# Kernel optimization log

Measured on AMD Instinct MI355X. Metric: run time of the kernel, lower is better.

## Reference

```python
import jax, jax.numpy as jnp
import numpy as np

N, C_IN, C_OUT, H, W = 64, 128, 128, 64, 64
K, RED = 3, 16


def setup_inputs() -> dict:
    key = jax.random.key(0)
    ks = jax.random.split(key, 12)
    s = 0.02
    return {
        "x": jax.random.normal(ks[0], (N, C_IN, H, W), dtype=jnp.float32),
        # spatial_extractor: Linear(16 -> 9)
        "W_sp": jax.random.normal(ks[1], (16, K * K), dtype=jnp.float32) * s,
        "b_sp": jnp.zeros((K * K,), dtype=jnp.float32),
        # out_channel_extractor: Linear(C_IN -> C_OUT//RED) -> ReLU -> Linear(-> C_OUT)
        "W_o1": jax.random.normal(ks[2], (C_IN, C_OUT // RED), dtype=jnp.float32) * s,
        "b_o1": jnp.zeros((C_OUT // RED,), dtype=jnp.float32),
        "W_o2": jax.random.normal(ks[3], (C_OUT // RED, C_OUT), dtype=jnp.float32) * s,
        "b_o2": jnp.zeros((C_OUT,), dtype=jnp.float32),
        # in_channel_extractor: Linear(C_IN -> C_IN//RED) -> ReLU -> Linear(-> C_IN)
        "W_i1": jax.random.normal(ks[4], (C_IN, C_IN // RED), dtype=jnp.float32) * s,
        "b_i1": jnp.zeros((C_IN // RED,), dtype=jnp.float32),
        "W_i2": jax.random.normal(ks[5], (C_IN // RED, C_IN), dtype=jnp.float32) * s,
        "b_i2": jnp.zeros((C_IN,), dtype=jnp.float32),
    }


def reference(x, W_sp, b_sp, W_o1, b_o1, W_o2, b_o2, W_i1, b_i1, W_i2, b_i2):
    n, c, h, w = x.shape
    # AdaptiveAvgPool2d(4): H,W divisible by 4 -> exact 16x16 mean pooling
    xs = x.reshape(n, c, 4, h // 4, 4, w // 4).mean(axis=(3, 5))  # [n,c,4,4]
    xs = xs.reshape(n, c, 16).mean(axis=1)                        # [n,16]
    sp = (xs @ W_sp + b_sp).reshape(n, K, K)                      # [n,3,3]
    gap = x.mean(axis=(2, 3))                                     # [n,C_in]
    co = jax.nn.relu(gap @ W_o1 + b_o1) @ W_o2 + b_o2             # [n,C_out]
    ci = jax.nn.relu(gap @ W_i1 + b_i1) @ W_i2 + b_i2             # [n,C_in]
    # per-sample kernel: [n, C_out, C_in, K, K]
    weight = (co[:, :, None, None, None] * ci[:, None, :, None, None]
              * sp[:, None, None, :, :])

    def per_sample_conv(xi, wi):
        # xi: [C_in,H,W], wi: [C_out,C_in,K,K]
        return jax.lax.conv_general_dilated(
            xi[None], wi, window_strides=(1, 1),
            padding=[(1, 1), (1, 1)])[0]

    return jax.vmap(per_sample_conv)(x, weight)  # [n,C_out,H,W]
```

## Files before the change

kernel.cpp:

```cpp
#include <hip/hip_runtime.h>

#define NB   64
#define CIN  128
#define COUT 128
#define HH   64
#define WW   64
#define HW   4096
#define HID  8


__global__ __launch_bounds__(256) void k_blocksums(const float* __restrict__ x,
                                                   float* __restrict__ bs) {
    const int plane = blockIdx.x;
    const int tid = threadIdx.x;
    const int r = tid >> 2;
    const int q = tid & 3;
    const float4* p = (const float4*)(x + (size_t)plane * HW + r * WW + q * 16);
    float4 a = p[0], b = p[1], c = p[2], d = p[3];
    float s = a.x + a.y + a.z + a.w + b.x + b.y + b.z + b.w
            + c.x + c.y + c.z + c.w + d.x + d.y + d.z + d.w;
    __shared__ float part[256];
    part[tid] = s;
    __syncthreads();
    if (tid < 16) {
        const int br = tid >> 2, qq = tid & 3;
        float acc = 0.0f;
        #pragma unroll
        for (int i = 0; i < 16; ++i) acc += part[(br * 16 + i) * 4 + qq];
        bs[plane * 16 + br * 4 + qq] = acc;
    }
}

__global__ __launch_bounds__(128) void k_coef(
    const float* __restrict__ bs,
    const float* __restrict__ W_sp, const float* __restrict__ b_sp,
    const float* __restrict__ W_o1, const float* __restrict__ b_o1,
    const float* __restrict__ W_o2, const float* __restrict__ b_o2,
    const float* __restrict__ W_i1, const float* __restrict__ b_i1,
    const float* __restrict__ W_i2, const float* __restrict__ b_i2,
    float* __restrict__ co, float* __restrict__ ci, float* __restrict__ sp)
{
    const int n = blockIdx.x, c = threadIdx.x;
    __shared__ float lbs[128][16];
    __shared__ float lgap[128];
    __shared__ float lxsm[16];
    __shared__ float lh[16];

    const float* src = bs + ((size_t)n * CIN + c) * 16;
    float s = 0.0f;
    #pragma unroll
    for (int j = 0; j < 16; ++j) { float v = src[j]; lbs[c][j] = v; s += v; }
    lgap[c] = s * (1.0f / 4096.0f);
    __syncthreads();

    if (c < 16) {
        float acc = 0.0f;
        for (int i = 0; i < 128; ++i) acc += lbs[i][c];
        lxsm[c] = acc * (1.0f / 32768.0f);
    }
    if (c < 8) {
        float acc = b_o1[c];
        for (int i = 0; i < 128; ++i) acc += lgap[i] * W_o1[i * 8 + c];
        lh[c] = fmaxf(acc, 0.0f);
    } else if (c < 16) {
        const int j = c - 8;
        float acc = b_i1[j];
        for (int i = 0; i < 128; ++i) acc += lgap[i] * W_i1[i * 8 + j];
        lh[c] = fmaxf(acc, 0.0f);
    }
    __syncthreads();

    float acco = b_o2[c];
    float acci = b_i2[c];
    #pragma unroll
    for (int j = 0; j < 8; ++j) {
        acco += lh[j]     * W_o2[j * 128 + c];
        acci += lh[8 + j] * W_i2[j * 128 + c];
    }
    co[n * COUT + c] = acco;
    ci[n * CIN + c]  = acci;

    if (c < 9) {
        float acc = b_sp[c];
        #pragma unroll
        for (int j = 0; j < 16; ++j) acc += lxsm[j] * W_sp[j * 9 + c];
        sp[n * 16 + c] = acc;
    }
}

__global__ __launch_bounds__(256) void k_t(const float* __restrict__ x,
                                           const float* __restrict__ ci,
                                           float* __restrict__ t) {
    const int bid = blockIdx.x;
    const int n = bid >> 2;
    const int y0 = (bid & 3) * 16;
    const int tid = threadIdx.x;
    const size_t base = (size_t)n * CIN * HW + (size_t)y0 * WW + (size_t)tid * 4;
    const float* cin = ci + n * CIN;

    float4 acc; acc.x = acc.y = acc.z = acc.w = 0.0f;
    for (int c = 0; c < CIN; c += 4) {
        float4 v0 = *(const float4*)(x + base + (size_t)(c + 0) * HW);
        float4 v1 = *(const float4*)(x + base + (size_t)(c + 1) * HW);
        float4 v2 = *(const float4*)(x + base + (size_t)(c + 2) * HW);
        float4 v3 = *(const float4*)(x + base + (size_t)(c + 3) * HW);
        const float c0 = cin[c], c1 = cin[c + 1], c2 = cin[c + 2], c3 = cin[c + 3];
        acc.x += v0.x * c0 + v1.x * c1 + v2.x * c2 + v3.x * c3;
        acc.y += v0.y * c0 + v1.y * c1 + v2.y * c2 + v3.y * c3;
        acc.z += v0.z * c0 + v1.z * c1 + v2.z * c2 + v3.z * c3;
        acc.w += v0.w * c0 + v1.w * c1 + v2.w * c2 + v3.w * c3;
    }
    *(float4*)(t + (size_t)n * HW + (size_t)y0 * WW + (size_t)tid * 4) = acc;
}

__global__ __launch_bounds__(256) void k_out(const float* __restrict__ t,
                                             const float* __restrict__ co,
                                             const float* __restrict__ sp,
                                             float* __restrict__ out) {
    const int bid = blockIdx.x;
    const int n = bid >> 3;
    const int y0 = (bid & 7) * 8;
    const int tid = threadIdx.x;

    __shared__ float ts[10][64];
    __shared__ float lco[128];
    __shared__ float lsp[9];

    if (tid < 128) lco[tid] = co[n * COUT + tid];
    if (tid < 9)  lsp[tid] = sp[n * 16 + tid];
    for (int k = tid; k < 640; k += 256) {
        const int ry = k >> 6, cx = k & 63;
        const int gy = y0 - 1 + ry;
        ts[ry][cx] = (gy >= 0 && gy < HH) ? t[(size_t)n * HW + gy * WW + cx] : 0.0f;
    }
    __syncthreads();

    const int i = tid & 127;
    const int row = i >> 4;
    const int c0 = (i & 15) * 4;
    float sv[4];
    #pragma unroll
    for (int u = 0; u < 4; ++u) {
        const int cc = c0 + u;
        float acc = 0.0f;
        #pragma unroll
        for (int dy = 0; dy < 3; ++dy) {
            #pragma unroll
            for (int dx = 0; dx < 3; ++dx) {
                const int cx = cc + dx - 1;
                if (cx >= 0 && cx < WW)
                    acc += lsp[dy * 3 + dx] * ts[row + dy][cx];
            }
        }
        sv[u] = acc;
    }

    const int ohalf = (tid >> 7) * 64;
    float4* outp = (float4*)(out + (size_t)n * COUT * HW + (size_t)y0 * WW) + i;
    #pragma unroll 4
    for (int op = 0; op < 64; ++op) {
        const int o = ohalf + op;
        const float scl = lco[o];
        float4 v; v.x = sv[0] * scl; v.y = sv[1] * scl; v.z = sv[2] * scl; v.w = sv[3] * scl;
        outp[(size_t)o * (HW / 4)] = v;
    }
}

extern "C" void kernel_launch(void* const* d_in, const int* in_sizes, int n_in,
                              void* d_out, int out_size, void* d_ws, size_t ws_size,
                              hipStream_t stream) {
    const float* x    = (const float*)d_in[0];
    const float* W_sp = (const float*)d_in[1];
    const float* b_sp = (const float*)d_in[2];
    const float* W_o1 = (const float*)d_in[3];
    const float* b_o1 = (const float*)d_in[4];
    const float* W_o2 = (const float*)d_in[5];
    const float* b_o2 = (const float*)d_in[6];
    const float* W_i1 = (const float*)d_in[7];
    const float* b_i1 = (const float*)d_in[8];
    const float* W_i2 = (const float*)d_in[9];
    const float* W_i2b= (const float*)d_in[10];

    float* ws = (float*)d_ws;
    float* bs = ws;
    float* co = ws + 131072;
    float* ci = ws + 139264;
    float* sp = ws + 147456;
    float* t  = ws + 148480;
    float* out = (float*)d_out;

    k_blocksums<<<NB * CIN, 256, 0, stream>>>(x, bs);
    k_coef<<<NB, 128, 0, stream>>>(bs, W_sp, b_sp, W_o1, b_o1, W_o2, b_o2,
                                   W_i1, b_i1, W_i2, W_i2b, co, ci, sp);
    k_t<<<NB * 4, 256, 0, stream>>>(x, ci, t);
    k_out<<<NB * 8, 256, 0, stream>>>(t, co, sp, out);
}
```

Measured before the change: 310.2 us.

## Fuse stats and channel reduction by projecting x onto W_i2 basis in one pass

```diff
diff --git a/kernel.cpp b/kernel.cpp
--- a/kernel.cpp
+++ b/kernel.cpp
@@ -6,28 +6,71 @@
 #define HH   64
 #define WW   64
 #define HW   4096
-#define HID  8
-
-
-__global__ __launch_bounds__(256) void k_blocksums(const float* __restrict__ x,
-                                                   float* __restrict__ bs) {
-    const int plane = blockIdx.x;
+
+typedef float f4v __attribute__((ext_vector_type(4)));
+
+
+__global__ __launch_bounds__(256) void k_stats(const float* __restrict__ x,
+                                               const float* __restrict__ W_i2,
+                                               const float* __restrict__ b_i2,
+                                               float* __restrict__ bs,
+                                               float* __restrict__ B) {
+    const int bid = blockIdx.x;
+    const int n  = bid >> 3;
+    const int rb = (bid >> 1) & 3;
+    const int p  = bid & 1;
+    const int c0 = p * 64;
     const int tid = threadIdx.x;
-    const int r = tid >> 2;
-    const int q = tid & 3;
-    const float4* p = (const float4*)(x + (size_t)plane * HW + r * WW + q * 16);
-    float4 a = p[0], b = p[1], c = p[2], d = p[3];
-    float s = a.x + a.y + a.z + a.w + b.x + b.y + b.z + b.w
-            + c.x + c.y + c.z + c.w + d.x + d.y + d.z + d.w;
-    __shared__ float part[256];
-    part[tid] = s;
-    __syncthreads();
-    if (tid < 16) {
-        const int br = tid >> 2, qq = tid & 3;
-        float acc = 0.0f;
-        #pragma unroll
-        for (int i = 0; i < 16; ++i) acc += part[(br * 16 + i) * 4 + qq];
-        bs[plane * 16 + br * 4 + qq] = acc;
+    const int r = tid >> 4;
+    const int colq = tid & 15;
+    const int y0 = rb * 16;
+
+    __shared__ float lw[9][64];
+    __shared__ float bsw[4][4][64];
+
+    if (tid < 64) {
+        lw[8][tid] = b_i2[c0 + tid];
+        #pragma unroll
+        for (int j = 0; j < 8; ++j) lw[j][tid] = W_i2[j * CIN + c0 + tid];
+    }
+    __syncthreads();
+
+    float4 acc[9];
+    #pragma unroll
+    for (int j = 0; j < 9; ++j) acc[j] = make_float4(0.f, 0.f, 0.f, 0.f);
+
+    const size_t xbase = ((size_t)n * CIN + c0) * HW + (size_t)(y0 + r) * WW + colq * 4;
+    const int wv = tid >> 6;
+    const int cb = colq >> 2;
+    const bool rep = (tid & 0x33) == 0;
+
+    for (int c = 0; c < 64; ++c) {
+        float4 v = *(const float4*)(x + xbase + (size_t)c * HW);
+        #pragma unroll
+        for (int j = 0; j < 9; ++j) {
+            const float w = lw[j][c];
+            acc[j].x += w * v.x; acc[j].y += w * v.y;
+            acc[j].z += w * v.z; acc[j].w += w * v.w;
+        }
+        float ls = (v.x + v.y) + (v.z + v.w);
+        ls += __shfl_xor(ls, 1,  64);
+        ls += __shfl_xor(ls, 2,  64);
+        ls += __shfl_xor(ls, 16, 64);
+        ls += __shfl_xor(ls, 32, 64);
+        if (rep) bsw[wv][cb][c] = ls;
+    }
+    __syncthreads();
+
+    {
+        const int c = tid >> 2, cb2 = tid & 3;
+        const float s = bsw[0][cb2][c] + bsw[1][cb2][c] + bsw[2][cb2][c] + bsw[3][cb2][c];
+        bs[((size_t)n * CIN + c0 + c) * 16 + rb * 4 + cb2] = s;
+    }
+
+    const size_t bpix = (size_t)(y0 + r) * WW + colq * 4;
+    #pragma unroll
+    for (int j = 0; j < 9; ++j) {
+        *(float4*)(B + ((size_t)(p * 9 + j) * NB + n) * HW + bpix) = acc[j];
     }
 }
 
@@ -37,11 +80,10 @@
     const float* __restrict__ W_o1, const float* __restrict__ b_o1,
     const float* __restrict__ W_o2, const float* __restrict__ b_o2,
     const float* __restrict__ W_i1, const float* __restrict__ b_i1,
-    const float* __restrict__ W_i2, const float* __restrict__ b_i2,
-    float* __restrict__ co, float* __restrict__ ci, float* __restrict__ sp)
+    float* __restrict__ co, float* __restrict__ hi, float* __restrict__ sp)
 {
     const int n = blockIdx.x, c = threadIdx.x;
-    __shared__ float lbs[128][16];
+    __shared__ float lbs[128][17];
     __shared__ float lgap[128];
     __shared__ float lxsm[16];
     __shared__ float lh[16];
@@ -49,7 +91,7 @@
     const float* src = bs + ((size_t)n * CIN + c) * 16;
     float s = 0.0f;
     #pragma unroll
-    for (int j = 0; j < 16; ++j) { float v = src[j]; lbs[c][j] = v; s += v; }
+    for (int j = 0; j < 16; ++j) { const float v = src[j]; lbs[c][j] = v; s += v; }
     lgap[c] = s * (1.0f / 4096.0f);
     __syncthreads();
 
@@ -71,15 +113,11 @@
     __syncthreads();
 
     float acco = b_o2[c];
-    float acci = b_i2[c];
-    #pragma unroll
-    for (int j = 0; j < 8; ++j) {
-        acco += lh[j]     * W_o2[j * 128 + c];
-        acci += lh[8 + j] * W_i2[j * 128 + c];
-    }
+    #pragma unroll
+    for (int j = 0; j < 8; ++j) acco += lh[j] * W_o2[j * 128 + c];
     co[n * COUT + c] = acco;
-    ci[n * CIN + c]  = acci;
-
+
+    if (c < 8) hi[n * 8 + c] = lh[8 + c];
     if (c < 9) {
         float acc = b_sp[c];
         #pragma unroll
@@ -88,60 +126,57 @@
     }
 }
 
-__global__ __launch_bounds__(256) void k_t(const float* __restrict__ x,
-                                           const float* __restrict__ ci,
-                                           float* __restrict__ t) {
-    const int bid = blockIdx.x;
-    const int n = bid >> 2;
-    const int y0 = (bid & 3) * 16;
-    const int tid = threadIdx.x;
-    const size_t base = (size_t)n * CIN * HW + (size_t)y0 * WW + (size_t)tid * 4;
-    const float* cin = ci + n * CIN;
-
-    float4 acc; acc.x = acc.y = acc.z = acc.w = 0.0f;
-    for (int c = 0; c < CIN; c += 4) {
-        float4 v0 = *(const float4*)(x + base + (size_t)(c + 0) * HW);
-        float4 v1 = *(const float4*)(x + base + (size_t)(c + 1) * HW);
-        float4 v2 = *(const float4*)(x + base + (size_t)(c + 2) * HW);
-        float4 v3 = *(const float4*)(x + base + (size_t)(c + 3) * HW);
-        const float c0 = cin[c], c1 = cin[c + 1], c2 = cin[c + 2], c3 = cin[c + 3];
-        acc.x += v0.x * c0 + v1.x * c1 + v2.x * c2 + v3.x * c3;
-        acc.y += v0.y * c0 + v1.y * c1 + v2.y * c2 + v3.y * c3;
-        acc.z += v0.z * c0 + v1.z * c1 + v2.z * c2 + v3.z * c3;
-        acc.w += v0.w * c0 + v1.w * c1 + v2.w * c2 + v3.w * c3;
-    }
-    *(float4*)(t + (size_t)n * HW + (size_t)y0 * WW + (size_t)tid * 4) = acc;
-}
-
-__global__ __launch_bounds__(256) void k_out(const float* __restrict__ t,
+__global__ __launch_bounds__(256) void k_out(const float* __restrict__ B,
                                              const float* __restrict__ co,
+                                             const float* __restrict__ hi,
                                              const float* __restrict__ sp,
                                              float* __restrict__ out) {
     const int bid = blockIdx.x;
-    const int n = bid >> 3;
+    const int n  = bid >> 3;
     const int y0 = (bid & 7) * 8;
     const int tid = threadIdx.x;
 
-    __shared__ float ts[10][64];
+    __shared__ float ts[10][66];
     __shared__ float lco[128];
     __shared__ float lsp[9];
+    __shared__ float lhi[8];
 
     if (tid < 128) lco[tid] = co[n * COUT + tid];
     if (tid < 9)  lsp[tid] = sp[n * 16 + tid];
-    for (int k = tid; k < 640; k += 256) {
-        const int ry = k >> 6, cx = k & 63;
+    if (tid < 8)  lhi[tid] = hi[n * 8 + tid];
+    __syncthreads();
+
+    if (tid < 160) {
+        const int ry = tid >> 4, cq = tid & 15;
         const int gy = y0 - 1 + ry;
-        ts[ry][cx] = (gy >= 0 && gy < HH) ? t[(size_t)n * HW + gy * WW + cx] : 0.0f;
+        float4 tv = make_float4(0.f, 0.f, 0.f, 0.f);
+        if (gy >= 0 && gy < HH) {
+            const size_t pix = (size_t)gy * WW + cq * 4;
+            const float* Bn = B + (size_t)n * HW + pix;
+            float4 a = *(const float4*)(Bn + (size_t)8  * NB * HW);
+            float4 b = *(const float4*)(Bn + (size_t)17 * NB * HW);
+            tv.x = a.x + b.x; tv.y = a.y + b.y; tv.z = a.z + b.z; tv.w = a.w + b.w;
+            #pragma unroll
+            for (int j = 0; j < 8; ++j) {
+                const float h = lhi[j];
+                float4 u = *(const float4*)(Bn + (size_t)j * NB * HW);
+                float4 w = *(const float4*)(Bn + (size_t)(9 + j) * NB * HW);
+                tv.x += h * (u.x + w.x); tv.y += h * (u.y + w.y);
+                tv.z += h * (u.z + w.z); tv.w += h * (u.w + w.w);
+            }
+        }
+        ts[ry][cq * 4 + 0] = tv.x; ts[ry][cq * 4 + 1] = tv.y;
+        ts[ry][cq * 4 + 2] = tv.z; ts[ry][cq * 4 + 3] = tv.w;
     }
     __syncthreads();
 
     const int i = tid & 127;
     const int row = i >> 4;
-    const int c0 = (i & 15) * 4;
+    const int cc0 = (i & 15) * 4;
     float sv[4];
     #pragma unroll
     for (int u = 0; u < 4; ++u) {
-        const int cc = c0 + u;
+        const int cc = cc0 + u;
         float acc = 0.0f;
         #pragma unroll
         for (int dy = 0; dy < 3; ++dy) {
@@ -156,13 +191,13 @@
     }
 
     const int ohalf = (tid >> 7) * 64;
-    float4* outp = (float4*)(out + (size_t)n * COUT * HW + (size_t)y0 * WW) + i;
+    float* outp = out + (size_t)n * COUT * HW + (size_t)y0 * WW + (size_t)i * 4;
     #pragma unroll 4
     for (int op = 0; op < 64; ++op) {
         const int o = ohalf + op;
         const float scl = lco[o];
-        float4 v; v.x = sv[0] * scl; v.y = sv[1] * scl; v.z = sv[2] * scl; v.w = sv[3] * scl;
-        outp[(size_t)o * (HW / 4)] = v;
+        f4v v; v.x = sv[0] * scl; v.y = sv[1] * scl; v.z = sv[2] * scl; v.w = sv[3] * scl;
+        __builtin_nontemporal_store(v, (f4v*)(outp + (size_t)o * HW));
     }
 }
 
@@ -179,19 +214,18 @@
     const float* W_i1 = (const float*)d_in[7];
     const float* b_i1 = (const float*)d_in[8];
     const float* W_i2 = (const float*)d_in[9];
-    const float* W_i2b= (const float*)d_in[10];
+    const float* b_i2 = (const float*)d_in[10];
 
     float* ws = (float*)d_ws;
     float* bs = ws;
     float* co = ws + 131072;
-    float* ci = ws + 139264;
-    float* sp = ws + 147456;
-    float* t  = ws + 148480;
+    float* hi = ws + 139264;
+    float* sp = ws + 139776;
+    float* B  = ws + 147456;
     float* out = (float*)d_out;
 
-    k_blocksums<<<NB * CIN, 256, 0, stream>>>(x, bs);
+    k_stats<<<NB * 8, 256, 0, stream>>>(x, W_i2, b_i2, bs, B);
     k_coef<<<NB, 128, 0, stream>>>(bs, W_sp, b_sp, W_o1, b_o1, W_o2, b_o2,
-                                   W_i1, b_i1, W_i2, W_i2b, co, ci, sp);
-    k_t<<<NB * 4, 256, 0, stream>>>(x, ci, t);
-    k_out<<<NB * 8, 256, 0, stream>>>(t, co, sp, out);
-}
+                                   W_i1, b_i1, co, hi, sp);
+    k_out<<<NB * 8, 256, 0, stream>>>(B, co, hi, sp, out);
+}
```

After: 284.4 us. -8.3%, faster.
